# Performance work log

Hardware: AMD Instinct MI355X
Metric: run time of the kernel (lower is better)

## Reference

```python
import jax, jax.numpy as jnp
import numpy as np

TOPK = 4  # hard-coded in the torch module


def setup_inputs() -> dict:
    key = jax.random.key(0)
    ks = jax.random.split(key, 7)
    B, S, D, H, E = 4, 1024, 2048, 2048, 8
    init = 0.02
    x = jax.random.normal(ks[0], (B, S, D), dtype=jnp.float32)
    Wg = jax.random.normal(ks[1], (D, E), dtype=jnp.float32) * init
    bg = jnp.zeros((E,), dtype=jnp.float32)
    W1 = jax.random.normal(ks[2], (E, D, H), dtype=jnp.float32) * init
    b1 = jnp.zeros((E, H), dtype=jnp.float32)
    W2 = jax.random.normal(ks[3], (E, H, D), dtype=jnp.float32) * init
    b2 = jnp.zeros((E, D), dtype=jnp.float32)
    return {"x": x, "Wg": Wg, "bg": bg, "W1": W1, "b1": b1, "W2": W2, "b2": b2}


def reference(x, Wg, bg, W1, b1, W2, b2):
    B, S, D = x.shape
    E = Wg.shape[1]
    xt = x.reshape(-1, D)  # [T, D], T = B*S

    # Routing: softmax in fp32, top-k, renormalize
    routing_logits = xt @ Wg + bg  # [T, E]
    probs = jax.nn.softmax(routing_logits.astype(jnp.float32), axis=-1)
    rw, sel = jax.lax.top_k(probs, TOPK)  # [T, K]
    rw = rw / jnp.sum(rw, axis=-1, keepdims=True)
    rw = rw.astype(x.dtype)

    # Per-token per-expert combine weight (0 for unselected experts): [T, E]
    comb = jnp.sum(jax.nn.one_hot(sel, E, dtype=x.dtype) * rw[..., None], axis=1)

    # Per-expert MLP: Linear -> exact GELU (torch default) -> Linear
    h = jax.nn.gelu(jnp.einsum('td,edh->teh', xt, W1) + b1, approximate=False)
    y = jnp.einsum('teh,ehd->ted', h, W2) + b2  # [T, E, D]

    # Weighted combine (scatter-add equivalent)
    final = jnp.einsum('ted,te->td', y, comb)
    return final.reshape(B, S, D), routing_logits
```

## Files before the change

### kernel.cpp

```cpp
#include <hip/hip_runtime.h>
#include <hip/hip_bf16.h>
#include <stdint.h>

#define T_TOK 4096
#define DDIM  2048
#define HDIM  2048
#define NEXP  8
#define NPAIR (T_TOK * 4)
#define NT    (DDIM / 64)
#define NITER (NT / 2)

typedef __attribute__((ext_vector_type(8))) short bf16x8;
typedef __attribute__((ext_vector_type(4))) float f32x4;
typedef __attribute__((ext_vector_type(4))) unsigned short u16x4v;
typedef __attribute__((ext_vector_type(8))) unsigned short u16x8v;

__device__ inline unsigned short f2bf(float f) {
  unsigned u = __builtin_bit_cast(unsigned, f);
  unsigned r = (u + 0x7fffu + ((u >> 16) & 1u)) >> 16;
  return (unsigned short)r;
}

__device__ inline float gelu_fast(float v) {
  float u = v + 0.044715f * v * v * v;
  return v / (1.0f + __expf(-1.59576912f * u));
}

__global__ __launch_bounds__(256) void transpose_conv_kernel(const float* __restrict__ W1,
                                                             const float* __restrict__ W2,
                                                             unsigned short* __restrict__ W1t,
                                                             unsigned short* __restrict__ W2t) {
  __shared__ float t2[64][129];
  int z = blockIdx.z;
  const float* src = (z < 8 ? W1 : W2) + (size_t)(z & 7) * DDIM * HDIM;
  unsigned short* dst = (z < 8 ? W1t : W2t) + (size_t)(z & 7) * DDIM * HDIM;
  int r0 = blockIdx.x * 128, c0 = blockIdx.y * 64;
  int tid = threadIdx.x;
  int lr = tid >> 4, lc = (tid & 15) * 4;
#pragma unroll
  for (int i = 0; i < 8; ++i) {
    float4 v = *(const float4*)(src + (size_t)(r0 + i * 16 + lr) * 2048 + c0 + lc);
    t2[lc + 0][i * 16 + lr] = v.x;
    t2[lc + 1][i * 16 + lr] = v.y;
    t2[lc + 2][i * 16 + lr] = v.z;
    t2[lc + 3][i * 16 + lr] = v.w;
  }
  __syncthreads();
  int sc = tid >> 4, rc = (tid & 15) * 8;
#pragma unroll
  for (int q = 0; q < 4; ++q) {
    int c = q * 16 + sc;
    u16x8v o;
#pragma unroll
    for (int k = 0; k < 8; ++k) o[k] = f2bf(t2[c][rc + k]);
    *(u16x8v*)(dst + (size_t)(c0 + c) * 2048 + r0 + rc) = o;
  }
}

__global__ __launch_bounds__(256) void routing_kernel(const float* __restrict__ x,
                                                      const float* __restrict__ Wg,
                                                      const float* __restrict__ bg,
                                                      float* __restrict__ logits,
                                                      float* __restrict__ rw,
                                                      int* __restrict__ sel,
                                                      unsigned short* __restrict__ xb) {
  int t = blockIdx.x * 4 + (threadIdx.x >> 6);
  int l = threadIdx.x & 63;
  const float* xr = x + (size_t)t * DDIM;
  float acc[8] = {0.f, 0.f, 0.f, 0.f, 0.f, 0.f, 0.f, 0.f};
#pragma unroll 1
  for (int i = 0; i < 8; ++i) {
    int d = i * 256 + l * 4;
    float4 xv = *(const float4*)(xr + d);
    u16x4v o;
    o[0] = f2bf(xv.x); o[1] = f2bf(xv.y); o[2] = f2bf(xv.z); o[3] = f2bf(xv.w);
    *(u16x4v*)(xb + (size_t)t * DDIM + d) = o;
    const float* wr = Wg + (size_t)d * 8;
    float xq[4] = {xv.x, xv.y, xv.z, xv.w};
#pragma unroll
    for (int q = 0; q < 4; ++q) {
      float4 w0 = *(const float4*)(wr + q * 8);
      float4 w1 = *(const float4*)(wr + q * 8 + 4);
      acc[0] = fmaf(xq[q], w0.x, acc[0]); acc[1] = fmaf(xq[q], w0.y, acc[1]);
      acc[2] = fmaf(xq[q], w0.z, acc[2]); acc[3] = fmaf(xq[q], w0.w, acc[3]);
      acc[4] = fmaf(xq[q], w1.x, acc[4]); acc[5] = fmaf(xq[q], w1.y, acc[5]);
      acc[6] = fmaf(xq[q], w1.z, acc[6]); acc[7] = fmaf(xq[q], w1.w, acc[7]);
    }
  }
#pragma unroll
  for (int e = 0; e < 8; ++e)
#pragma unroll
    for (int off = 32; off > 0; off >>= 1) acc[e] += __shfl_down(acc[e], off);
  if (l == 0) {
    float lg[8];
#pragma unroll
    for (int e = 0; e < 8; ++e) {
      lg[e] = acc[e] + bg[e];
      logits[(size_t)t * 8 + e] = lg[e];
    }
    float mx = lg[0];
#pragma unroll
    for (int e = 1; e < 8; ++e) mx = fmaxf(mx, lg[e]);
    float p[8];
#pragma unroll
    for (int e = 0; e < 8; ++e) p[e] = expf(lg[e] - mx);
    bool used[8] = {false, false, false, false, false, false, false, false};
    float wsum = 0.f; int se[4]; float pv[4];
    for (int k = 0; k < 4; ++k) {
      int best = 0; float bv = -1.f;
      for (int e = 0; e < 8; ++e)
        if (!used[e] && p[e] > bv) { bv = p[e]; best = e; }
      used[best] = true; se[k] = best; pv[k] = bv; wsum += bv;
    }
    for (int k = 0; k < 4; ++k) {
      rw[t * 4 + k] = pv[k] / wsum;
      sel[t * 4 + k] = se[k];
    }
  }
}

__global__ __launch_bounds__(256) void hist_kernel(const int* __restrict__ sel,
                                                   int* __restrict__ blkcnt) {
  __shared__ int h[NEXP];
  if (threadIdx.x < NEXP) h[threadIdx.x] = 0;
  __syncthreads();
  int t = blockIdx.x * 256 + threadIdx.x;
#pragma unroll
  for (int k = 0; k < 4; ++k) atomicAdd(&h[sel[t * 4 + k]], 1);
  __syncthreads();
  if (threadIdx.x < NEXP) blkcnt[blockIdx.x * NEXP + threadIdx.x] = h[threadIdx.x];
}

__global__ void plan_kernel(const int* __restrict__ blkcnt, int* __restrict__ cnt,
                            int* __restrict__ off, int* __restrict__ base) {
  if (threadIdx.x == 0) {
    int c[NEXP];
    for (int e = 0; e < NEXP; ++e) c[e] = 0;
    for (int b = 0; b < 16; ++b)
      for (int e = 0; e < NEXP; ++e) { base[b * NEXP + e] = c[e]; c[e] += blkcnt[b * NEXP + e]; }
    int s = 0;
    for (int e = 0; e < NEXP; ++e) { cnt[e] = c[e]; off[e] = s; s += c[e]; }
  }
}

__global__ __launch_bounds__(256) void fill_kernel(const int* __restrict__ sel,
                                                   const float* __restrict__ rw,
                                                   const int* __restrict__ off,
                                                   const int* __restrict__ base,
                                                   int* __restrict__ tok,
                                                   float* __restrict__ wof) {
  __shared__ int h[NEXP];
  if (threadIdx.x < NEXP) h[threadIdx.x] = 0;
  __syncthreads();
  int t = blockIdx.x * 256 + threadIdx.x;
#pragma unroll
  for (int k = 0; k < 4; ++k) {
    int e = sel[t * 4 + k];
    int r = atomicAdd(&h[e], 1);
    int p = off[e] + base[blockIdx.x * NEXP + e] + r;
    tok[p] = t;
    wof[p] = rw[t * 4 + k];
  }
}

#define GLL(g, l) __builtin_amdgcn_global_load_lds(                         \
    (const __attribute__((address_space(1))) void*)(g),                    \
    (__attribute__((address_space(3))) void*)(l), 16, 0, 0)

#define BARX { __builtin_amdgcn_s_barrier(); __builtin_amdgcn_sched_barrier(0); }
#define WAIT4 { asm volatile("s_waitcnt vmcnt(4)" ::: "memory"); __builtin_amdgcn_sched_barrier(0); }
#define WAIT8 { asm volatile("s_waitcnt vmcnt(8)" ::: "memory"); __builtin_amdgcn_sched_barrier(0); }
#define WAIT0 { asm volatile("s_waitcnt vmcnt(0)" ::: "memory"); __builtin_amdgcn_sched_barrier(0); }

#define ST_A0(b, ko) { GLL(aP[0] + (ko), ldsc + (b)*65536 +     0 + stDst); GLL(aP[1] + (ko), ldsc + (b)*65536 +  8192 + stDst); }
#define ST_A1(b, ko) { GLL(aP[2] + (ko), ldsc + (b)*65536 + 16384 + stDst); GLL(aP[3] + (ko), ldsc + (b)*65536 + 24576 + stDst); }
#define ST_B0(b, ko) { GLL(bP[0] + (ko), ldsc + (b)*65536 + 32768 + stDst); GLL(bP[1] + (ko), ldsc + (b)*65536 + 40960 + stDst); }
#define ST_B1(b, ko) { GLL(bP[2] + (ko), ldsc + (b)*65536 + 49152 + stDst); GLL(bP[3] + (ko), ldsc + (b)*65536 + 57344 + stDst); }

#define RD_A(Ab, mq) { _Pragma("unroll") for (int i_ = 0; i_ < 4; ++i_) { \
    af[i_][0] = *(const bf16x8*)&(Ab)[((size_t)(wrlr + ((mq)*4 + i_)*16))*64 + c0]; \
    af[i_][1] = *(const bf16x8*)&(Ab)[((size_t)(wrlr + ((mq)*4 + i_)*16))*64 + c1]; } }
#define RD_B(Bb, nq) { _Pragma("unroll") for (int j_ = 0; j_ < 2; ++j_) { \
    bfr[(nq)*2 + j_][0] = *(const bf16x8*)&(Bb)[((size_t)(wclr + ((nq)*2 + j_)*16))*64 + c0]; \
    bfr[(nq)*2 + j_][1] = *(const bf16x8*)&(Bb)[((size_t)(wclr + ((nq)*2 + j_)*16))*64 + c1]; } }
#define MMA_Q(mq, nq) { __builtin_amdgcn_s_setprio(1); \
  _Pragma("unroll") for (int kk_ = 0; kk_ < 2; ++kk_) \
  _Pragma("unroll") for (int i_ = 0; i_ < 4; ++i_) \
  _Pragma("unroll") for (int j_ = 0; j_ < 2; ++j_) \
    acc[(mq)*4 + i_][(nq)*2 + j_] = __builtin_amdgcn_mfma_f32_16x16x32_bf16( \
        af[i_][kk_], bfr[(nq)*2 + j_][kk_], acc[(mq)*4 + i_][(nq)*2 + j_], 0, 0, 0); \
  __builtin_amdgcn_s_setprio(0); }

__global__ __launch_bounds__(512, 2) void gemm1_kernel(
    const unsigned short* __restrict__ A, const unsigned short* __restrict__ Bt,
    const float* __restrict__ bias, const int* __restrict__ cnt,
    const int* __restrict__ off, const int* __restrict__ tok,
    unsigned short* __restrict__ hout) {
  __shared__ unsigned short lds[65536];
  const int bid = blockIdx.x;
  const int e   = bid & 7;
  const int rem = bid >> 3;
  const int bm  = rem & 15;
  const int bn  = rem >> 4;
  const int ne  = cnt[e];
  const int m0  = bm * 256;
  if (m0 >= ne) return;
  const int oe  = off[e];
  const int n0  = bn * 256;
  const int tid = threadIdx.x;
  const int w   = tid >> 6;
  const int l   = tid & 63;

  const int srow = tid >> 3;
  const int scg  = ((tid & 7) ^ (srow & 7)) * 8;
  const unsigned short* aP[4];
  const unsigned short* bP[4];
#pragma unroll
  for (int j = 0; j < 4; ++j) {
    int r = m0 + j * 64 + srow;
    if (r > ne - 1) r = ne - 1;
    aP[j] = A + (size_t)tok[oe + r] * 2048 + scg;
    bP[j] = Bt + ((size_t)e * 2048 + n0 + j * 64 + srow) * 2048 + scg;
  }
  char* ldsc = (char*)lds;
  const int stDst = tid * 16;

  const int wr = (w >> 2) * 128;
  const int wc = (w & 3) * 64;
  const int lr = l & 15;
  const int lq = l >> 4;
  const int cx = lr & 7;
  const int wrlr = wr + lr;
  const int wclr = wc + lr;
  const int c0 = ((0 * 4 + lq) ^ cx) * 8;
  const int c1 = ((1 * 4 + lq) ^ cx) * 8;

  const unsigned short* Ab0 = lds;
  const unsigned short* Bb0 = lds + 16384;
  const unsigned short* Ab1 = lds + 32768;
  const unsigned short* Bb1 = lds + 49152;

  f32x4 acc[8][4];
#pragma unroll
  for (int m = 0; m < 8; ++m)
#pragma unroll
    for (int n = 0; n < 4; ++n) acc[m][n] = (f32x4){0.f, 0.f, 0.f, 0.f};

  ST_B0(0, 0); ST_B1(0, 0); ST_A0(0, 0); ST_A1(0, 0);
  ST_B0(1, 64); ST_B1(1, 64);
  WAIT4; BARX;

#pragma unroll 1
  for (int it = 0; it < NITER; ++it) {
    const int ko1 = (2 * it + 1) * 64;
    const int ko2 = (2 * it + 2) * 64;
    const int ko3 = (2 * it + 3) * 64;
    const bool pf = (it < NITER - 1);
    bf16x8 af[4][2], bfr[4][2];

    ST_A0(1, ko1);
    RD_A(Ab0, 0); RD_B(Bb0, 0);
    MMA_Q(0, 0); BARX;
    ST_A1(1, ko1);
    RD_B(Bb0, 1);
    MMA_Q(0, 1); BARX;
    if (pf) ST_B0(0, ko2);
    RD_A(Ab0, 1);
    MMA_Q(1, 0); BARX;
    if (pf) ST_B1(0, ko2);
    MMA_Q(1, 1);
    if (pf) { WAIT4; } else { WAIT0; }
    BARX;
    if (pf) ST_A0(0, ko2);
    RD_A(Ab1, 0); RD_B(Bb1, 0);
    MMA_Q(0, 0); BARX;
    if (pf) ST_A1(0, ko2);
    RD_B(Bb1, 1);
    MMA_Q(0, 1); BARX;
    if (pf) ST_B0(1, ko3);
    RD_A(Ab1, 1);
    MMA_Q(1, 0); BARX;
    if (pf) ST_B1(1, ko3);
    MMA_Q(1, 1);
    if (pf) { WAIT4; }
    BARX;
  }

  const int rj = lq * 4;
  float bvn[4];
#pragma unroll
  for (int n = 0; n < 4; ++n) bvn[n] = bias[e * 2048 + n0 + wc + n * 16 + lr];
#pragma unroll
  for (int m = 0; m < 8; ++m) {
    const int rbase = m0 + wr + m * 16 + rj;
#pragma unroll
    for (int j = 0; j < 4; ++j) {
      const int row = rbase + j;
      if (row < ne) {
#pragma unroll
        for (int n = 0; n < 4; ++n) {
          const int col = n0 + wc + n * 16 + lr;
          float v = acc[m][n][j] + bvn[n];
          hout[(size_t)(oe + row) * 2048 + col] = f2bf(gelu_fast(v));
        }
      }
    }
  }
}

__global__ __launch_bounds__(256) void gemm2_kernel(
    const unsigned short* __restrict__ A, const unsigned short* __restrict__ Bt,
    const float* __restrict__ bias, const int* __restrict__ cnt,
    const int* __restrict__ off, const int* __restrict__ tok,
    const float* __restrict__ wof, float* __restrict__ out) {
  __shared__ unsigned short lds[32768];
  const int bid = blockIdx.x;
  const int e   = bid & 7;
  const int rem = bid >> 3;
  const int bm  = rem & 31;
  const int bn  = rem >> 5;
  const int ne  = cnt[e];
  const int m0  = bm * 128;
  if (m0 >= ne) return;
  const int oe  = off[e];
  const int n0  = bn * 128;
  const int tid = threadIdx.x;
  const int w   = tid >> 6;
  const int l   = tid & 63;

  const int srow = tid >> 3;
  const int scg  = ((tid & 7) ^ (srow & 7)) * 8;
  const unsigned short* aP[4];
  const unsigned short* bP[4];
#pragma unroll
  for (int j = 0; j < 4; ++j) {
    int r = m0 + j * 32 + srow;
    if (r > ne - 1) r = ne - 1;
    aP[j] = A + (size_t)(oe + r) * 2048 + scg;
    bP[j] = Bt + ((size_t)e * 2048 + n0 + j * 32 + srow) * 2048 + scg;
  }
  char* ldsc = (char*)lds;
  const int stDst = tid * 16;

  const int wr = (w >> 1) * 64;
  const int wc = (w & 1) * 64;
  const int lr = l & 15;
  const int lq = l >> 4;
  const int cx = lr & 7;
  const int wrlr = wr + lr;
  const int wclr = wc + lr;
  const int c0 = ((0 * 4 + lq) ^ cx) * 8;
  const int c1 = ((1 * 4 + lq) ^ cx) * 8;

  f32x4 acc[4][4];
#pragma unroll
  for (int m = 0; m < 4; ++m)
#pragma unroll
    for (int n = 0; n < 4; ++n) acc[m][n] = (f32x4){0.f, 0.f, 0.f, 0.f};

#pragma unroll
  for (int j = 0; j < 4; ++j) GLL(aP[j], ldsc + j * 4096 + stDst);
#pragma unroll
  for (int j = 0; j < 4; ++j) GLL(bP[j], ldsc + 16384 + j * 4096 + stDst);

#pragma unroll 1
  for (int t = 0; t < NT; ++t) {
    if (t < NT - 1) {
      const int ko = (t + 1) * 64;
      char* dstA = ldsc + ((t + 1) & 1) * 32768;
#pragma unroll
      for (int j = 0; j < 4; ++j) GLL(aP[j] + ko, dstA + j * 4096 + stDst);
#pragma unroll
      for (int j = 0; j < 4; ++j) GLL(bP[j] + ko, dstA + 16384 + j * 4096 + stDst);
      WAIT8;
    } else {
      WAIT0;
    }
    __builtin_amdgcn_s_barrier();

    const unsigned short* Ab = lds + (t & 1) * 16384;
    const unsigned short* Bb = Ab + 8192;
    bf16x8 af[4][2], bfr[4][2];
#pragma unroll
    for (int m = 0; m < 4; ++m) {
      af[m][0] = *(const bf16x8*)&Ab[(size_t)(wrlr + m * 16) * 64 + c0];
      af[m][1] = *(const bf16x8*)&Ab[(size_t)(wrlr + m * 16) * 64 + c1];
    }
#pragma unroll
    for (int n = 0; n < 4; ++n) {
      bfr[n][0] = *(const bf16x8*)&Bb[(size_t)(wclr + n * 16) * 64 + c0];
      bfr[n][1] = *(const bf16x8*)&Bb[(size_t)(wclr + n * 16) * 64 + c1];
    }
    __builtin_amdgcn_s_setprio(1);
#pragma unroll
    for (int kk = 0; kk < 2; ++kk)
#pragma unroll
      for (int m = 0; m < 4; ++m)
#pragma unroll
        for (int n = 0; n < 4; ++n)
          acc[m][n] = __builtin_amdgcn_mfma_f32_16x16x32_bf16(af[m][kk], bfr[n][kk], acc[m][n], 0, 0, 0);
    __builtin_amdgcn_s_setprio(0);
    __builtin_amdgcn_s_barrier();
  }

  const int rj = lq * 4;
  float bvn[4];
#pragma unroll
  for (int n = 0; n < 4; ++n) bvn[n] = bias[e * 2048 + n0 + wc + n * 16 + lr];
#pragma unroll
  for (int m = 0; m < 4; ++m) {
    const int rbase = m0 + wr + m * 16 + rj;
#pragma unroll
    for (int j = 0; j < 4; ++j) {
      const int row = rbase + j;
      if (row < ne) {
        const int p = oe + row;
        const int tk = tok[p];
        const float wf = wof[p];
#pragma unroll
        for (int n = 0; n < 4; ++n) {
          const int col = n0 + wc + n * 16 + lr;
          atomicAdd(&out[(size_t)tk * 2048 + col], wf * (acc[m][n][j] + bvn[n]));
        }
      }
    }
  }
}

extern "C" void kernel_launch(void* const* d_in, const int* in_sizes, int n_in,
                              void* d_out, int out_size, void* d_ws, size_t ws_size,
                              hipStream_t stream) {
  const float* x  = (const float*)d_in[0];
  const float* Wg = (const float*)d_in[1];
  const float* bg = (const float*)d_in[2];
  const float* W1 = (const float*)d_in[3];
  const float* b1 = (const float*)d_in[4];
  const float* W2 = (const float*)d_in[5];
  const float* b2 = (const float*)d_in[6];
  float* out = (float*)d_out;
  float* logits = out + (size_t)T_TOK * DDIM;

  char* ws = (char*)d_ws;
  int* cnt    = (int*)(ws);
  int* off    = (int*)(ws + 64);
  int* blkcnt = (int*)(ws + 128);
  int* base   = (int*)(ws + 768);
  size_t o = 2048;
  unsigned short* xb   = (unsigned short*)(ws + o); o += (size_t)T_TOK * DDIM * 2;
  unsigned short* W1t  = (unsigned short*)(ws + o); o += (size_t)NEXP * DDIM * HDIM * 2;
  unsigned short* W2t  = (unsigned short*)(ws + o); o += (size_t)NEXP * DDIM * HDIM * 2;
  unsigned short* hbuf = (unsigned short*)(ws + o); o += (size_t)NPAIR * HDIM * 2;
  float* rw  = (float*)(ws + o); o += (size_t)T_TOK * 4 * 4;
  int*   sel = (int*)(ws + o);   o += (size_t)T_TOK * 4 * 4;
  int*   tok = (int*)(ws + o);   o += (size_t)NPAIR * 4;
  float* wof = (float*)(ws + o); o += (size_t)NPAIR * 4;

  hipMemsetAsync(d_out, 0, (size_t)T_TOK * DDIM * sizeof(float), stream);

  transpose_conv_kernel<<<dim3(16, 32, 16), 256, 0, stream>>>(W1, W2, W1t, W2t);
  routing_kernel<<<T_TOK / 4, 256, 0, stream>>>(x, Wg, bg, logits, rw, sel, xb);
  hist_kernel<<<16, 256, 0, stream>>>(sel, blkcnt);
  plan_kernel<<<1, 64, 0, stream>>>(blkcnt, cnt, off, base);
  fill_kernel<<<16, 256, 0, stream>>>(sel, rw, off, base, tok, wof);

  gemm1_kernel<<<dim3(1024), 512, 0, stream>>>(xb, W1t, b1, cnt, off, tok, hbuf);
  gemm2_kernel<<<dim3(4096), 256, 0, stream>>>(hbuf, W2t, b2, cnt, off, tok, wof, out);
}
```

Before: 506.3 us.

## Enlarge gemm2 block tile to 256x256 with 128x128 per-wave subtiles

```diff
diff --git a/kernel.cpp b/kernel.cpp
--- a/kernel.cpp
+++ b/kernel.cpp
@@ -169,7 +169,7 @@
 
 #define BARX { __builtin_amdgcn_s_barrier(); __builtin_amdgcn_sched_barrier(0); }
 #define WAIT4 { asm volatile("s_waitcnt vmcnt(4)" ::: "memory"); __builtin_amdgcn_sched_barrier(0); }
-#define WAIT8 { asm volatile("s_waitcnt vmcnt(8)" ::: "memory"); __builtin_amdgcn_sched_barrier(0); }
+#define WAIT16 { asm volatile("s_waitcnt vmcnt(16)" ::: "memory"); __builtin_amdgcn_sched_barrier(0); }
 #define WAIT0 { asm volatile("s_waitcnt vmcnt(0)" ::: "memory"); __builtin_amdgcn_sched_barrier(0); }
 
 #define ST_A0(b, ko) { GLL(aP[0] + (ko), ldsc + (b)*65536 +     0 + stDst); GLL(aP[1] + (ko), ldsc + (b)*65536 +  8192 + stDst); }
@@ -308,42 +308,41 @@
   }
 }
 
-__global__ __launch_bounds__(256) void gemm2_kernel(
+__global__ __launch_bounds__(256, 1) void gemm2_kernel(
     const unsigned short* __restrict__ A, const unsigned short* __restrict__ Bt,
     const float* __restrict__ bias, const int* __restrict__ cnt,
     const int* __restrict__ off, const int* __restrict__ tok,
     const float* __restrict__ wof, float* __restrict__ out) {
-  __shared__ unsigned short lds[32768];
+  __shared__ unsigned short lds[65536];
   const int bid = blockIdx.x;
   const int e   = bid & 7;
   const int rem = bid >> 3;
-  const int bm  = rem & 31;
-  const int bn  = rem >> 5;
+  const int bm  = rem & 15;
+  const int bn  = rem >> 4;
   const int ne  = cnt[e];
-  const int m0  = bm * 128;
+  const int m0  = bm * 256;
   if (m0 >= ne) return;
   const int oe  = off[e];
-  const int n0  = bn * 128;
+  const int n0  = bn * 256;
   const int tid = threadIdx.x;
   const int w   = tid >> 6;
   const int l   = tid & 63;
 
   const int srow = tid >> 3;
   const int scg  = ((tid & 7) ^ (srow & 7)) * 8;
-  const unsigned short* aP[4];
-  const unsigned short* bP[4];
-#pragma unroll
-  for (int j = 0; j < 4; ++j) {
+  const unsigned short* aP[8];
+#pragma unroll
+  for (int j = 0; j < 8; ++j) {
     int r = m0 + j * 32 + srow;
     if (r > ne - 1) r = ne - 1;
     aP[j] = A + (size_t)(oe + r) * 2048 + scg;
-    bP[j] = Bt + ((size_t)e * 2048 + n0 + j * 32 + srow) * 2048 + scg;
-  }
+  }
+  const unsigned short* bP = Bt + ((size_t)e * 2048 + n0 + srow) * 2048 + scg;
   char* ldsc = (char*)lds;
   const int stDst = tid * 16;
 
-  const int wr = (w >> 1) * 64;
-  const int wc = (w & 1) * 64;
+  const int wr = (w >> 1) * 128;
+  const int wc = (w & 1) * 128;
   const int lr = l & 15;
   const int lq = l >> 4;
   const int cx = lr & 7;
@@ -352,63 +351,61 @@
   const int c0 = ((0 * 4 + lq) ^ cx) * 8;
   const int c1 = ((1 * 4 + lq) ^ cx) * 8;
 
-  f32x4 acc[4][4];
-#pragma unroll
-  for (int m = 0; m < 4; ++m)
-#pragma unroll
-    for (int n = 0; n < 4; ++n) acc[m][n] = (f32x4){0.f, 0.f, 0.f, 0.f};
-
-#pragma unroll
-  for (int j = 0; j < 4; ++j) GLL(aP[j], ldsc + j * 4096 + stDst);
-#pragma unroll
-  for (int j = 0; j < 4; ++j) GLL(bP[j], ldsc + 16384 + j * 4096 + stDst);
+  f32x4 acc[8][8];
+#pragma unroll
+  for (int m = 0; m < 8; ++m)
+#pragma unroll
+    for (int n = 0; n < 8; ++n) acc[m][n] = (f32x4){0.f, 0.f, 0.f, 0.f};
+
+#pragma unroll
+  for (int j = 0; j < 8; ++j) GLL(aP[j], ldsc + j * 4096 + stDst);
+#pragma unroll
+  for (int j = 0; j < 8; ++j) GLL(bP + j * 65536, ldsc + 32768 + j * 4096 + stDst);
 
 #pragma unroll 1
   for (int t = 0; t < NT; ++t) {
     if (t < NT - 1) {
       const int ko = (t + 1) * 64;
-      char* dstA = ldsc + ((t + 1) & 1) * 32768;
-#pragma unroll
-      for (int j = 0; j < 4; ++j) GLL(aP[j] + ko, dstA + j * 4096 + stDst);
-#pragma unroll
-      for (int j = 0; j < 4; ++j) GLL(bP[j] + ko, dstA + 16384 + j * 4096 + stDst);
-      WAIT8;
+      char* d = ldsc + ((t + 1) & 1) * 65536;
+#pragma unroll
+      for (int j = 0; j < 8; ++j) GLL(aP[j] + ko, d + j * 4096 + stDst);
+#pragma unroll
+      for (int j = 0; j < 8; ++j) GLL(bP + j * 65536 + ko, d + 32768 + j * 4096 + stDst);
+      WAIT16;
     } else {
       WAIT0;
     }
-    __builtin_amdgcn_s_barrier();
-
-    const unsigned short* Ab = lds + (t & 1) * 16384;
-    const unsigned short* Bb = Ab + 8192;
-    bf16x8 af[4][2], bfr[4][2];
-#pragma unroll
-    for (int m = 0; m < 4; ++m) {
-      af[m][0] = *(const bf16x8*)&Ab[(size_t)(wrlr + m * 16) * 64 + c0];
-      af[m][1] = *(const bf16x8*)&Ab[(size_t)(wrlr + m * 16) * 64 + c1];
-    }
-#pragma unroll
-    for (int n = 0; n < 4; ++n) {
-      bfr[n][0] = *(const bf16x8*)&Bb[(size_t)(wclr + n * 16) * 64 + c0];
-      bfr[n][1] = *(const bf16x8*)&Bb[(size_t)(wclr + n * 16) * 64 + c1];
-    }
-    __builtin_amdgcn_s_setprio(1);
-#pragma unroll
-    for (int kk = 0; kk < 2; ++kk)
-#pragma unroll
-      for (int m = 0; m < 4; ++m)
-#pragma unroll
-        for (int n = 0; n < 4; ++n)
-          acc[m][n] = __builtin_amdgcn_mfma_f32_16x16x32_bf16(af[m][kk], bfr[n][kk], acc[m][n], 0, 0, 0);
-    __builtin_amdgcn_s_setprio(0);
-    __builtin_amdgcn_s_barrier();
+    BARX;
+
+    const unsigned short* Ab = lds + (t & 1) * 32768;
+    const unsigned short* Bb = Ab + 16384;
+#pragma unroll
+    for (int kk = 0; kk < 2; ++kk) {
+      const int cs = kk ? c1 : c0;
+      bf16x8 af[8], bfr[8];
+#pragma unroll
+      for (int m = 0; m < 8; ++m)
+        af[m] = *(const bf16x8*)&Ab[(size_t)(wrlr + m * 16) * 64 + cs];
+#pragma unroll
+      for (int n = 0; n < 8; ++n)
+        bfr[n] = *(const bf16x8*)&Bb[(size_t)(wclr + n * 16) * 64 + cs];
+      __builtin_amdgcn_s_setprio(1);
+#pragma unroll
+      for (int m = 0; m < 8; ++m)
+#pragma unroll
+        for (int n = 0; n < 8; ++n)
+          acc[m][n] = __builtin_amdgcn_mfma_f32_16x16x32_bf16(af[m], bfr[n], acc[m][n], 0, 0, 0);
+      __builtin_amdgcn_s_setprio(0);
+    }
+    BARX;
   }
 
   const int rj = lq * 4;
-  float bvn[4];
-#pragma unroll
-  for (int n = 0; n < 4; ++n) bvn[n] = bias[e * 2048 + n0 + wc + n * 16 + lr];
-#pragma unroll
-  for (int m = 0; m < 4; ++m) {
+  float bvn[8];
+#pragma unroll
+  for (int n = 0; n < 8; ++n) bvn[n] = bias[e * 2048 + n0 + wc + n * 16 + lr];
+#pragma unroll
+  for (int m = 0; m < 8; ++m) {
     const int rbase = m0 + wr + m * 16 + rj;
 #pragma unroll
     for (int j = 0; j < 4; ++j) {
@@ -418,7 +415,7 @@
         const int tk = tok[p];
         const float wf = wof[p];
 #pragma unroll
-        for (int n = 0; n < 4; ++n) {
+        for (int n = 0; n < 8; ++n) {
           const int col = n0 + wc + n * 16 + lr;
           atomicAdd(&out[(size_t)tk * 2048 + col], wf * (acc[m][n][j] + bvn[n]));
         }
@@ -464,5 +461,5 @@
   fill_kernel<<<16, 256, 0, stream>>>(sel, rw, off, base, tok, wof);
 
   gemm1_kernel<<<dim3(1024), 512, 0, stream>>>(xb, W1t, b1, cnt, off, tok, hbuf);
-  gemm2_kernel<<<dim3(4096), 256, 0, stream>>>(hbuf, W2t, b2, cnt, off, tok, wof, out);
-}
+  gemm2_kernel<<<dim3(1024), 256, 0, stream>>>(hbuf, W2t, b2, cnt, off, tok, wof, out);
+}
```

After: 803.2 us. 1.59x slower.
